# Performance work log

Hardware: AMD Instinct MI355X
Metric: run time of the kernel (lower is better)

The kernel has to match this reference:

```python
import jax, jax.numpy as jnp
import numpy as np

TEMPERATURE = 0.5
B, D = 4096, 256


def setup_inputs() -> dict:
    key = jax.random.key(0)
    k1, k2 = jax.random.split(key)
    z_i = jax.random.normal(k1, (B, D), dtype=jnp.float32)
    z_j = jax.random.normal(k2, (B, D), dtype=jnp.float32)
    return {"z_i": z_i, "z_j": z_j}


def reference(z_i, z_j):
    batch = z_i.shape[0]
    n = 2 * batch
    z = jnp.concatenate([z_i, z_j], axis=0)                      # [2B, D]
    z = z / jnp.linalg.norm(z, axis=1, keepdims=True)            # L2-normalize rows
    # cosine_similarity of unit vectors == dot product -> single GEMM
    sim = jnp.einsum('id,jd->ij', z, z) / TEMPERATURE            # [2B, 2B]
    mask = jnp.eye(n, dtype=bool)
    sim = jnp.where(mask, -jnp.inf, sim)                         # mask self-similarity
    positives = jnp.concatenate(
        [jnp.diagonal(sim, offset=batch), jnp.diagonal(sim, offset=-batch)], axis=0
    )                                                            # [2B]
    loss = -positives + jax.nn.logsumexp(sim, axis=1)            # [2B]
    return loss.mean()
```

## Files before the change

kernel.cpp:

```cpp
#include <hip/hip_runtime.h>
#include <hip/hip_bf16.h>
#include <stdint.h>
#include <stddef.h>


#define B_ROWS 4096
#define D_DIM  256
#define N_ROWS 8192
#define BM 128
#define BN 64

typedef __bf16 bf16;
typedef bf16  bf16x8  __attribute__((ext_vector_type(8)));
typedef bf16  bf16x4  __attribute__((ext_vector_type(4)));
typedef float floatx4 __attribute__((ext_vector_type(4)));

__global__ __launch_bounds__(256) void normalize_kernel(
    const float* __restrict__ z_i, const float* __restrict__ z_j,
    bf16* __restrict__ zn, float* __restrict__ sumexp) {
  const int wave = threadIdx.x >> 6;
  const int lane = threadIdx.x & 63;
  const int row  = blockIdx.x * 4 + wave;
  const float* src = (row < B_ROWS) ? (z_i + (size_t)row * D_DIM)
                                    : (z_j + (size_t)(row - B_ROWS) * D_DIM);
  float4 v = ((const float4*)src)[lane];
  float ss = v.x * v.x + v.y * v.y + v.z * v.z + v.w * v.w;
  #pragma unroll
  for (int m = 1; m < 64; m <<= 1) ss += __shfl_xor(ss, m);
  const float rn = rsqrtf(ss) * 1.6986436f;
  bf16x4 o;
  o[0] = (bf16)(v.x * rn);
  o[1] = (bf16)(v.y * rn);
  o[2] = (bf16)(v.z * rn);
  o[3] = (bf16)(v.w * rn);
  ((bf16x4*)(zn + (size_t)row * D_DIM))[lane] = o;
  if (lane == 0) sumexp[row] = 0.f;
}

__global__ __launch_bounds__(256, 2) void simexp_kernel(
    const bf16* __restrict__ zn, float* __restrict__ sumexp,
    float* __restrict__ pos) {
  __shared__ __align__(16) bf16 Bs[2][BN * D_DIM];

  const int tid   = threadIdx.x;
  const int wave  = tid >> 6;
  const int lane  = tid & 63;
  const int lcol  = lane & 15;
  const int lquad = lane >> 4;
  const int wr = (wave >> 1) * 64;
  const int wc = (wave & 1) * 32;
  const int ri = blockIdx.x >> 3;
  const int cj = blockIdx.x & 7;
  const int row_base = ri * BM;
  const int niter = (ri < 32 && cj >= 6) ? 9 : 8;

  auto jt64 = [&](int t) {
    const int s   = (t == 8) ? 32 : 4 * cj + (t >> 1);
    const int sub = (t == 8) ? (cj - 6) : (t & 1);
    return 2 * ((ri + s) & 63) + sub;
  };

  auto stage = [&](int buf, const bf16* src) {
    #pragma unroll
    for (int it = 0; it < 8; ++it) {
      const int s   = it * 256 + tid;
      const int n   = s >> 5;
      const int kcs = s & 31;
      const int kc  = (kcs & 24) | ((kcs & 7) ^ (n & 7));
      __builtin_amdgcn_global_load_lds(
          (const __attribute__((address_space(1))) unsigned int*)
              (src + (size_t)n * D_DIM + kc * 8),
          (__attribute__((address_space(3))) unsigned int*)&Bs[buf][s * 8],
          16, 0, 0);
    }
  };

  stage(0, zn + (size_t)row_base * D_DIM);
  stage(1, zn + (size_t)(row_base + 64) * D_DIM);
  __syncthreads();

  floatx4 af[4][8];
  {
    const int half = wr >> 6;
    #pragma unroll
    for (int ti = 0; ti < 4; ++ti) {
      const int n = ti * 16 + lcol;
      #pragma unroll
      for (int kq = 0; kq < 8; ++kq) {
        const int kc  = kq * 4 + lquad;
        const int kcs = (kc & 24) | ((kc & 7) ^ (n & 7));
        af[ti][kq] = *(const floatx4*)(&Bs[half][(n * 32 + kcs) * 8]);
      }
    }
  }
  __syncthreads();

  stage(0, zn + (size_t)jt64(0) * BN * D_DIM);

  float rowsum[4][4];
  #pragma unroll
  for (int ti = 0; ti < 4; ++ti)
    #pragma unroll
    for (int r = 0; r < 4; ++r) rowsum[ti][r] = 0.f;

  #pragma unroll 1
  for (int t = 0; t < niter; ++t) {
    __syncthreads();
    if (t + 1 < niter) stage((t + 1) & 1, zn + (size_t)jt64(t + 1) * BN * D_DIM);

    floatx4 acc[4][2];
    #pragma unroll
    for (int ti = 0; ti < 4; ++ti)
      #pragma unroll
      for (int tj = 0; tj < 2; ++tj) acc[ti][tj] = floatx4{0.f, 0.f, 0.f, 0.f};

    const bf16* bbase = &Bs[t & 1][0];
    #pragma unroll
    for (int kq = 0; kq < 8; ++kq) {
      const int kc  = kq * 4 + lquad;
      bf16x8 bfr[2];
      #pragma unroll
      for (int tj = 0; tj < 2; ++tj) {
        const int n   = wc + tj * 16 + lcol;
        const int kcs = (kc & 24) | ((kc & 7) ^ (n & 7));
        bfr[tj] = *(const bf16x8*)(bbase + n * D_DIM + kcs * 8);
      }
      #pragma unroll
      for (int ti = 0; ti < 4; ++ti)
        #pragma unroll
        for (int tj = 0; tj < 2; ++tj)
          acc[ti][tj] = __builtin_amdgcn_mfma_f32_16x16x32_bf16(
              __builtin_bit_cast(bf16x8, af[ti][kq]), bfr[tj], acc[ti][tj],
              0, 0, 0);
    }

    const int s    = (t == 8) ? 32 : 4 * cj + (t >> 1);
    const bool diag = (s == 0);
    const bool posT = (s == 32);
    const int jt = jt64(t);
    const int col_base = jt * BN;
    float colsum[2] = {0.f, 0.f};
    #pragma unroll
    for (int ti = 0; ti < 4; ++ti) {
      #pragma unroll
      for (int tj = 0; tj < 2; ++tj) {
        #pragma unroll
        for (int r = 0; r < 4; ++r) {
          const float v = acc[ti][tj][r];
          float e = __builtin_amdgcn_exp2f(v);
          if (diag || posT) {
            const int rg = row_base + wr + ti * 16 + lquad * 4 + r;
            const int cg = col_base + wc + tj * 16 + lcol;
            if (diag && cg == rg) e = 0.f;
            if (posT && cg == rg + B_ROWS) {
              const float p = v * 0.6931471805599453f;
              pos[rg] = p;
              pos[cg] = p;
            }
          }
          rowsum[ti][r] += e;
          colsum[tj]    += e;
        }
      }
    }

    if (!diag) {
      #pragma unroll
      for (int tj = 0; tj < 2; ++tj) {
        float cs = colsum[tj];
        cs += __shfl_xor(cs, 16);
        cs += __shfl_xor(cs, 32);
        if (lquad == 0)
          atomicAdd(&sumexp[col_base + wc + tj * 16 + lcol], cs);
      }
    }
  }

  #pragma unroll
  for (int ti = 0; ti < 4; ++ti) {
    #pragma unroll
    for (int r = 0; r < 4; ++r) {
      float s2 = rowsum[ti][r];
      s2 += __shfl_xor(s2, 1);
      s2 += __shfl_xor(s2, 2);
      s2 += __shfl_xor(s2, 4);
      s2 += __shfl_xor(s2, 8);
      if (lcol == 0) {
        const int grow = row_base + wr + ti * 16 + lquad * 4 + r;
        atomicAdd(&sumexp[grow], s2);
      }
    }
  }
}

__global__ __launch_bounds__(1024) void reduce_kernel(
    const float* __restrict__ sumexp, const float* __restrict__ pos,
    float* __restrict__ out) {
  __shared__ float ws[16];
  const int tid = threadIdx.x;
  float s = 0.f;
  const float ln2 = 0.6931471805599453f;
  for (int k = tid; k < N_ROWS; k += 1024)
    s += __builtin_amdgcn_logf(sumexp[k]) * ln2 - pos[k];
  #pragma unroll
  for (int m = 1; m < 64; m <<= 1) s += __shfl_xor(s, m);
  const int wave = tid >> 6, lane = tid & 63;
  if (lane == 0) ws[wave] = s;
  __syncthreads();
  if (wave == 0) {
    float t = (lane < 16) ? ws[lane] : 0.f;
    #pragma unroll
    for (int m = 1; m < 16; m <<= 1) t += __shfl_xor(t, m);
    if (lane == 0) out[0] = t * (1.0f / N_ROWS);
  }
}

extern "C" void kernel_launch(void* const* d_in, const int* in_sizes, int n_in,
                              void* d_out, int out_size, void* d_ws,
                              size_t ws_size, hipStream_t stream) {
  const float* z_i = (const float*)d_in[0];
  const float* z_j = (const float*)d_in[1];
  float* out = (float*)d_out;

  bf16* zn = (bf16*)d_ws;
  float* sumexp = (float*)((char*)d_ws + (size_t)N_ROWS * D_DIM * sizeof(bf16));
  float* pos = sumexp + N_ROWS;

  normalize_kernel<<<N_ROWS / 4, 256, 0, stream>>>(z_i, z_j, zn, sumexp);
  simexp_kernel<<<512, 256, 0, stream>>>(zn, sumexp, pos);
  reduce_kernel<<<1, 1024, 0, stream>>>(sumexp, pos, out);
}
```

Baseline: 95.57 us.

## Enlarge column tiles to 128 with 8-wave blocks and phased staging pipeline

Result: faster. 92.55 us (-3.2%).

```diff
diff --git a/kernel.cpp b/kernel.cpp
--- a/kernel.cpp
+++ b/kernel.cpp
@@ -8,7 +8,7 @@
 #define D_DIM  256
 #define N_ROWS 8192
 #define BM 128
-#define BN 64
+#define BN 128
 
 typedef __bf16 bf16;
 typedef bf16  bf16x8  __attribute__((ext_vector_type(8)));
@@ -37,7 +37,7 @@
   if (lane == 0) sumexp[row] = 0.f;
 }
 
-__global__ __launch_bounds__(256, 2) void simexp_kernel(
+__global__ __launch_bounds__(512, 2) void simexp_kernel(
     const bf16* __restrict__ zn, float* __restrict__ sumexp,
     float* __restrict__ pos) {
   __shared__ __align__(16) bf16 Bs[2][BN * D_DIM];
@@ -47,23 +47,18 @@
   const int lane  = tid & 63;
   const int lcol  = lane & 15;
   const int lquad = lane >> 4;
-  const int wr = (wave >> 1) * 64;
-  const int wc = (wave & 1) * 32;
-  const int ri = blockIdx.x >> 3;
-  const int cj = blockIdx.x & 7;
+  const int wr = (wave >> 2) * 64;
+  const int wc = (wave & 3) * 32;
+  const int ri = blockIdx.x >> 2;
+  const int cj = blockIdx.x & 3;
   const int row_base = ri * BM;
-  const int niter = (ri < 32 && cj >= 6) ? 9 : 8;
-
-  auto jt64 = [&](int t) {
-    const int s   = (t == 8) ? 32 : 4 * cj + (t >> 1);
-    const int sub = (t == 8) ? (cj - 6) : (t & 1);
-    return 2 * ((ri + s) & 63) + sub;
-  };
-
-  auto stage = [&](int buf, const bf16* src) {
-    #pragma unroll
-    for (int it = 0; it < 8; ++it) {
-      const int s   = it * 256 + tid;
+  const bool has_tail = (ri < 32 && cj >= 2);
+
+  auto ct_of = [&](int t) { return (ri + 8 * cj + t) & 63; };
+
+  auto stageB = [&](int buf, const bf16* src, int it0, int it1) {
+    for (int it = it0; it < it1; ++it) {
+      const int s   = it * 512 + tid;
       const int n   = s >> 5;
       const int kcs = s & 31;
       const int kc  = (kcs & 24) | ((kcs & 7) ^ (n & 7));
@@ -75,70 +70,94 @@
     }
   };
 
-  stage(0, zn + (size_t)row_base * D_DIM);
-  stage(1, zn + (size_t)(row_base + 64) * D_DIM);
+  stageB(0, zn + (size_t)row_base * D_DIM, 0, 8);
+  stageB(1, zn + (size_t)ct_of(0) * BM * D_DIM, 0, 8);
   __syncthreads();
 
   floatx4 af[4][8];
-  {
-    const int half = wr >> 6;
-    #pragma unroll
-    for (int ti = 0; ti < 4; ++ti) {
-      const int n = ti * 16 + lcol;
-      #pragma unroll
-      for (int kq = 0; kq < 8; ++kq) {
-        const int kc  = kq * 4 + lquad;
-        const int kcs = (kc & 24) | ((kc & 7) ^ (n & 7));
-        af[ti][kq] = *(const floatx4*)(&Bs[half][(n * 32 + kcs) * 8]);
-      }
-    }
-  }
-  __syncthreads();
-
-  stage(0, zn + (size_t)jt64(0) * BN * D_DIM);
-
-  float rowsum[4][4];
-  #pragma unroll
-  for (int ti = 0; ti < 4; ++ti)
-    #pragma unroll
-    for (int r = 0; r < 4; ++r) rowsum[ti][r] = 0.f;
-
-  #pragma unroll 1
-  for (int t = 0; t < niter; ++t) {
-    __syncthreads();
-    if (t + 1 < niter) stage((t + 1) & 1, zn + (size_t)jt64(t + 1) * BN * D_DIM);
-
-    floatx4 acc[4][2];
-    #pragma unroll
-    for (int ti = 0; ti < 4; ++ti)
-      #pragma unroll
-      for (int tj = 0; tj < 2; ++tj) acc[ti][tj] = floatx4{0.f, 0.f, 0.f, 0.f};
-
-    const bf16* bbase = &Bs[t & 1][0];
+  #pragma unroll
+  for (int ti = 0; ti < 4; ++ti) {
+    const int n = wr + ti * 16 + lcol;
     #pragma unroll
     for (int kq = 0; kq < 8; ++kq) {
       const int kc  = kq * 4 + lquad;
-      bf16x8 bfr[2];
-      #pragma unroll
-      for (int tj = 0; tj < 2; ++tj) {
-        const int n   = wc + tj * 16 + lcol;
-        const int kcs = (kc & 24) | ((kc & 7) ^ (n & 7));
-        bfr[tj] = *(const bf16x8*)(bbase + n * D_DIM + kcs * 8);
-      }
-      #pragma unroll
-      for (int ti = 0; ti < 4; ++ti)
-        #pragma unroll
-        for (int tj = 0; tj < 2; ++tj)
-          acc[ti][tj] = __builtin_amdgcn_mfma_f32_16x16x32_bf16(
-              __builtin_bit_cast(bf16x8, af[ti][kq]), bfr[tj], acc[ti][tj],
-              0, 0, 0);
-    }
-
-    const int s    = (t == 8) ? 32 : 4 * cj + (t >> 1);
-    const bool diag = (s == 0);
-    const bool posT = (s == 32);
-    const int jt = jt64(t);
-    const int col_base = jt * BN;
+      const int kcs = (kc & 24) | ((kc & 7) ^ (n & 7));
+      af[ti][kq] = *(const floatx4*)(&Bs[0][(n * 32 + kcs) * 8]);
+    }
+  }
+  __syncthreads();
+
+  float rowsum[4][4];
+  #pragma unroll
+  for (int ti = 0; ti < 4; ++ti)
+    #pragma unroll
+    for (int r = 0; r < 4; ++r) rowsum[ti][r] = 0.f;
+
+#define MFMA_(A, B_, C) __builtin_amdgcn_mfma_f32_16x16x32_bf16( \
+    __builtin_bit_cast(bf16x8, A), B_, C, 0, 0, 0)
+#define PHASE(KQA, KQB, IT0, IT1, DO_VM)                                  \
+  {                                                                       \
+    bf16x8 bfrA[2], bfrB[2];                                              \
+    const int kcA = (KQA) * 4 + lquad, kcB = (KQB) * 4 + lquad;           \
+    _Pragma("unroll")                                                     \
+    for (int tj = 0; tj < 2; ++tj) {                                      \
+      const int n  = wc + tj * 16 + lcol;                                 \
+      const int sA = (kcA & 24) | ((kcA & 7) ^ (n & 7));                  \
+      const int sB = (kcB & 24) | ((kcB & 7) ^ (n & 7));                  \
+      bfrA[tj] = *(const bf16x8*)(bbase + n * D_DIM + sA * 8);            \
+      bfrB[tj] = *(const bf16x8*)(bbase + n * D_DIM + sB * 8);            \
+    }                                                                     \
+    stageB(sb, nsrc, IT0, IT1);                                           \
+    __builtin_amdgcn_sched_barrier(0);                                    \
+    __builtin_amdgcn_s_barrier();                                         \
+    asm volatile("s_waitcnt lgkmcnt(0)" ::: "memory");                    \
+    __builtin_amdgcn_sched_barrier(0);                                    \
+    __builtin_amdgcn_s_setprio(1);                                        \
+    _Pragma("unroll")                                                     \
+    for (int ti = 0; ti < 4; ++ti) {                                      \
+      acc[ti][0] = MFMA_(af[ti][KQA], bfrA[0], acc[ti][0]);               \
+      acc[ti][1] = MFMA_(af[ti][KQA], bfrA[1], acc[ti][1]);               \
+    }                                                                     \
+    _Pragma("unroll")                                                     \
+    for (int ti = 0; ti < 4; ++ti) {                                      \
+      acc[ti][0] = MFMA_(af[ti][KQB], bfrB[0], acc[ti][0]);               \
+      acc[ti][1] = MFMA_(af[ti][KQB], bfrB[1], acc[ti][1]);               \
+    }                                                                     \
+    __builtin_amdgcn_s_setprio(0);                                        \
+    if (DO_VM) asm volatile("s_waitcnt vmcnt(0)" ::: "memory");           \
+    __builtin_amdgcn_sched_barrier(0);                                    \
+    __builtin_amdgcn_s_barrier();                                         \
+  }
+
+  #pragma unroll 1
+  for (int t = 0; t < 8; ++t) {
+    const int cb = (t ^ 1) & 1;
+    const int sb = cb ^ 1;
+    const bf16* bbase = &Bs[cb][0];
+    const bf16* nsrc = nullptr;
+    int nl = 0;
+    if (t < 7) {
+      nsrc = zn + (size_t)ct_of(t + 1) * BM * D_DIM;
+      nl = 8;
+    } else if (has_tail) {
+      nsrc = zn + (size_t)((ri + 32) * BM + (cj - 2) * 64) * D_DIM;
+      nl = 4;
+    }
+    const int nh = nl >> 1;
+
+    floatx4 acc[4][2];
+    #pragma unroll
+    for (int ti = 0; ti < 4; ++ti)
+      #pragma unroll
+      for (int tj = 0; tj < 2; ++tj) acc[ti][tj] = floatx4{0.f, 0.f, 0.f, 0.f};
+
+    PHASE(0, 1, 0, nh, false)
+    PHASE(2, 3, nh, nl, false)
+    PHASE(4, 5, 0, 0, false)
+    PHASE(6, 7, 0, 0, true)
+
+    const bool diag = (cj == 0 && t == 0);
+    const int col_base = ct_of(t) * BM;
     float colsum[2] = {0.f, 0.f};
     #pragma unroll
     for (int ti = 0; ti < 4; ++ti) {
@@ -148,22 +167,16 @@
         for (int r = 0; r < 4; ++r) {
           const float v = acc[ti][tj][r];
           float e = __builtin_amdgcn_exp2f(v);
-          if (diag || posT) {
+          if (diag) {
             const int rg = row_base + wr + ti * 16 + lquad * 4 + r;
             const int cg = col_base + wc + tj * 16 + lcol;
-            if (diag && cg == rg) e = 0.f;
-            if (posT && cg == rg + B_ROWS) {
-              const float p = v * 0.6931471805599453f;
-              pos[rg] = p;
-              pos[cg] = p;
-            }
+            if (cg == rg) e = 0.f;
           }
           rowsum[ti][r] += e;
           colsum[tj]    += e;
         }
       }
     }
-
     if (!diag) {
       #pragma unroll
       for (int tj = 0; tj < 2; ++tj) {
@@ -175,6 +188,64 @@
       }
     }
   }
+
+  if (has_tail && wc < 64) {
+    const int h = cj - 2;
+    const int col_base = (ri + 32) * BM + h * 64;
+    const bf16* bbase = &Bs[1][0];
+    floatx4 acc[4][2];
+    #pragma unroll
+    for (int ti = 0; ti < 4; ++ti)
+      #pragma unroll
+      for (int tj = 0; tj < 2; ++tj) acc[ti][tj] = floatx4{0.f, 0.f, 0.f, 0.f};
+    #pragma unroll
+    for (int kq = 0; kq < 8; ++kq) {
+      const int kc = kq * 4 + lquad;
+      bf16x8 bfr[2];
+      #pragma unroll
+      for (int tj = 0; tj < 2; ++tj) {
+        const int n   = wc + tj * 16 + lcol;
+        const int kcs = (kc & 24) | ((kc & 7) ^ (n & 7));
+        bfr[tj] = *(const bf16x8*)(bbase + n * D_DIM + kcs * 8);
+      }
+      #pragma unroll
+      for (int ti = 0; ti < 4; ++ti) {
+        acc[ti][0] = MFMA_(af[ti][kq], bfr[0], acc[ti][0]);
+        acc[ti][1] = MFMA_(af[ti][kq], bfr[1], acc[ti][1]);
+      }
+    }
+    float colsum[2] = {0.f, 0.f};
+    #pragma unroll
+    for (int ti = 0; ti < 4; ++ti) {
+      #pragma unroll
+      for (int tj = 0; tj < 2; ++tj) {
+        #pragma unroll
+        for (int r = 0; r < 4; ++r) {
+          const float v = acc[ti][tj][r];
+          const float e = __builtin_amdgcn_exp2f(v);
+          const int rg = row_base + wr + ti * 16 + lquad * 4 + r;
+          const int cg = col_base + wc + tj * 16 + lcol;
+          if (cg == rg + B_ROWS) {
+            const float p = v * 0.6931471805599453f;
+            pos[rg] = p;
+            pos[cg] = p;
+          }
+          rowsum[ti][r] += e;
+          colsum[tj]    += e;
+        }
+      }
+    }
+    #pragma unroll
+    for (int tj = 0; tj < 2; ++tj) {
+      float cs = colsum[tj];
+      cs += __shfl_xor(cs, 16);
+      cs += __shfl_xor(cs, 32);
+      if (lquad == 0)
+        atomicAdd(&sumexp[col_base + wc + tj * 16 + lcol], cs);
+    }
+  }
+#undef PHASE
+#undef MFMA_
 
   #pragma unroll
   for (int ti = 0; ti < 4; ++ti) {
@@ -227,6 +298,6 @@
   float* pos = sumexp + N_ROWS;
 
   normalize_kernel<<<N_ROWS / 4, 256, 0, stream>>>(z_i, z_j, zn, sumexp);
-  simexp_kernel<<<512, 256, 0, stream>>>(zn, sumexp, pos);
+  simexp_kernel<<<256, 512, 0, stream>>>(zn, sumexp, pos);
   reduce_kernel<<<1, 1024, 0, stream>>>(sumexp, pos, out);
 }
```

## Use 128x128 tiles with 8 waves and software-pipeline MFMA against exp epilogue

Applied to the files above, without the earlier changes.

Result: faster. 92.08 us (-3.7%).

```diff
diff --git a/kernel.cpp b/kernel.cpp
--- a/kernel.cpp
+++ b/kernel.cpp
@@ -8,7 +8,7 @@
 #define D_DIM  256
 #define N_ROWS 8192
 #define BM 128
-#define BN 64
+#define BN 128
 
 typedef __bf16 bf16;
 typedef bf16  bf16x8  __attribute__((ext_vector_type(8)));
@@ -37,7 +37,7 @@
   if (lane == 0) sumexp[row] = 0.f;
 }
 
-__global__ __launch_bounds__(256, 2) void simexp_kernel(
+__global__ __launch_bounds__(512, 2) void simexp_kernel(
     const bf16* __restrict__ zn, float* __restrict__ sumexp,
     float* __restrict__ pos) {
   __shared__ __align__(16) bf16 Bs[2][BN * D_DIM];
@@ -47,23 +47,18 @@
   const int lane  = tid & 63;
   const int lcol  = lane & 15;
   const int lquad = lane >> 4;
-  const int wr = (wave >> 1) * 64;
-  const int wc = (wave & 1) * 32;
-  const int ri = blockIdx.x >> 3;
-  const int cj = blockIdx.x & 7;
+  const int wr = (wave >> 1) * 32;
+  const int wc = (wave & 1) * 64;
+  const int ri = blockIdx.x >> 2;
+  const int cj = blockIdx.x & 3;
   const int row_base = ri * BM;
-  const int niter = (ri < 32 && cj >= 6) ? 9 : 8;
-
-  auto jt64 = [&](int t) {
-    const int s   = (t == 8) ? 32 : 4 * cj + (t >> 1);
-    const int sub = (t == 8) ? (cj - 6) : (t & 1);
-    return 2 * ((ri + s) & 63) + sub;
-  };
-
-  auto stage = [&](int buf, const bf16* src) {
-    #pragma unroll
-    for (int it = 0; it < 8; ++it) {
-      const int s   = it * 256 + tid;
+  const bool has_tail = (ri < 32 && cj >= 2);
+
+  auto ct_of = [&](int t) { return (ri + 8 * cj + t) & 63; };
+
+  auto stageB = [&](int buf, const bf16* src, int it0, int it1) {
+    for (int it = it0; it < it1; ++it) {
+      const int s   = it * 512 + tid;
       const int n   = s >> 5;
       const int kcs = s & 31;
       const int kc  = (kcs & 24) | ((kcs & 7) ^ (n & 7));
@@ -75,109 +70,142 @@
     }
   };
 
-  stage(0, zn + (size_t)row_base * D_DIM);
-  stage(1, zn + (size_t)(row_base + 64) * D_DIM);
+  stageB(0, zn + (size_t)row_base * D_DIM, 0, 8);
+  stageB(1, zn + (size_t)ct_of(0) * BM * D_DIM, 0, 8);
   __syncthreads();
 
-  floatx4 af[4][8];
-  {
-    const int half = wr >> 6;
-    #pragma unroll
-    for (int ti = 0; ti < 4; ++ti) {
-      const int n = ti * 16 + lcol;
-      #pragma unroll
-      for (int kq = 0; kq < 8; ++kq) {
-        const int kc  = kq * 4 + lquad;
-        const int kcs = (kc & 24) | ((kc & 7) ^ (n & 7));
-        af[ti][kq] = *(const floatx4*)(&Bs[half][(n * 32 + kcs) * 8]);
-      }
-    }
-  }
-  __syncthreads();
-
-  stage(0, zn + (size_t)jt64(0) * BN * D_DIM);
-
-  float rowsum[4][4];
-  #pragma unroll
-  for (int ti = 0; ti < 4; ++ti)
-    #pragma unroll
-    for (int r = 0; r < 4; ++r) rowsum[ti][r] = 0.f;
-
-  #pragma unroll 1
-  for (int t = 0; t < niter; ++t) {
-    __syncthreads();
-    if (t + 1 < niter) stage((t + 1) & 1, zn + (size_t)jt64(t + 1) * BN * D_DIM);
-
-    floatx4 acc[4][2];
-    #pragma unroll
-    for (int ti = 0; ti < 4; ++ti)
-      #pragma unroll
-      for (int tj = 0; tj < 2; ++tj) acc[ti][tj] = floatx4{0.f, 0.f, 0.f, 0.f};
-
-    const bf16* bbase = &Bs[t & 1][0];
+  floatx4 af[2][8];
+  #pragma unroll
+  for (int ti = 0; ti < 2; ++ti) {
+    const int n = wr + ti * 16 + lcol;
     #pragma unroll
     for (int kq = 0; kq < 8; ++kq) {
       const int kc  = kq * 4 + lquad;
-      bf16x8 bfr[2];
+      const int kcs = (kc & 24) | ((kc & 7) ^ (n & 7));
+      af[ti][kq] = *(const floatx4*)(&Bs[0][(n * 32 + kcs) * 8]);
+    }
+  }
+  __syncthreads();
+
+  float rowsum[2][4];
+  #pragma unroll
+  for (int ti = 0; ti < 2; ++ti)
+    #pragma unroll
+    for (int r = 0; r < 4; ++r) rowsum[ti][r] = 0.f;
+
+#define MFMA_(A, B_, C) __builtin_amdgcn_mfma_f32_16x16x32_bf16( \
+    __builtin_bit_cast(bf16x8, A), B_, C, 0, 0, 0)
+
+#define QPHASE(ACC, Q)                                                    \
+  {                                                                       \
+    bf16x8 bfr[8];                                                        \
+    const int n = wc + (Q) * 16 + lcol;                                   \
+    _Pragma("unroll")                                                     \
+    for (int kq = 0; kq < 8; ++kq) {                                      \
+      const int kc  = kq * 4 + lquad;                                     \
+      const int kcs = (kc & 24) | ((kc & 7) ^ (n & 7));                   \
+      bfr[kq] = *(const bf16x8*)(bbase + n * D_DIM + kcs * 8);            \
+    }                                                                     \
+    ACC[0] = floatx4{0.f, 0.f, 0.f, 0.f};                                 \
+    ACC[1] = floatx4{0.f, 0.f, 0.f, 0.f};                                 \
+    _Pragma("unroll")                                                     \
+    for (int kq = 0; kq < 8; ++kq) {                                      \
+      ACC[0] = MFMA_(af[0][kq], bfr[kq], ACC[0]);                         \
+      ACC[1] = MFMA_(af[1][kq], bfr[kq], ACC[1]);                         \
+    }                                                                     \
+  }
+
+#define SLICE(ACC, Q, CB, DG)                                             \
+  {                                                                       \
+    float cs = 0.f;                                                       \
+    _Pragma("unroll")                                                     \
+    for (int ti = 0; ti < 2; ++ti) {                                      \
+      _Pragma("unroll")                                                   \
+      for (int r = 0; r < 4; ++r) {                                       \
+        const float v = ACC[ti][r];                                       \
+        float e = __builtin_amdgcn_exp2f(v);                              \
+        if (DG) {                                                         \
+          const int rg = row_base + wr + ti * 16 + lquad * 4 + r;         \
+          const int cg = (CB) + wc + (Q) * 16 + lcol;                     \
+          if (cg == rg) e = 0.f;                \
+        }                                                                 \
+        rowsum[ti][r] += e;                                               \
+        cs += e;                                                          \
+      }                                                                   \
+    }                                                                     \
+    cs += __shfl_xor(cs, 16);                                             \
+    cs += __shfl_xor(cs, 32);                                             \
+    if (!(DG) && lquad == 0)                                              \
+      atomicAdd(&sumexp[(CB) + wc + (Q) * 16 + lcol], cs);                \
+  }
+
+  floatx4 a3[2];
+  int  pcol3  = 0;
+  bool pdiag3 = false;
+
+  #pragma unroll 1
+  for (int t = 0; t < 8; ++t) {
+    const bf16* bbase = &Bs[(t + 1) & 1][0];
+    const int sb = t & 1;
+    if (t < 7) {
+      stageB(sb, zn + (size_t)ct_of(t + 1) * BM * D_DIM, 0, 8);
+    } else if (has_tail) {
+      stageB(sb, zn + (size_t)((ri + 32) * BM + (cj - 2) * 64) * D_DIM, 0, 4);
+    }
+    const int  colb = ct_of(t) * BM;
+    const bool diag = (cj == 0 && t == 0);
+
+    floatx4 a0[2], a1[2], a2[2];
+    QPHASE(a0, 0)
+    if (t > 0) SLICE(a3, 3, pcol3, pdiag3)
+    QPHASE(a1, 1)
+    SLICE(a0, 0, colb, diag)
+    QPHASE(a2, 2)
+    SLICE(a1, 1, colb, diag)
+    QPHASE(a3, 3)
+    SLICE(a2, 2, colb, diag)
+    pcol3 = colb;
+    pdiag3 = diag;
+    __syncthreads();
+  }
+  SLICE(a3, 3, pcol3, pdiag3)
+
+  if (has_tail && wc == 0) {
+    const int colb = (ri + 32) * BM + (cj - 2) * 64;
+    const bf16* bbase = &Bs[1][0];
+    floatx4 ta[2];
+    #pragma unroll
+    for (int Q = 0; Q < 4; ++Q) {
+      QPHASE(ta, Q)
+      float cs = 0.f;
       #pragma unroll
-      for (int tj = 0; tj < 2; ++tj) {
-        const int n   = wc + tj * 16 + lcol;
-        const int kcs = (kc & 24) | ((kc & 7) ^ (n & 7));
-        bfr[tj] = *(const bf16x8*)(bbase + n * D_DIM + kcs * 8);
-      }
-      #pragma unroll
-      for (int ti = 0; ti < 4; ++ti)
-        #pragma unroll
-        for (int tj = 0; tj < 2; ++tj)
-          acc[ti][tj] = __builtin_amdgcn_mfma_f32_16x16x32_bf16(
-              __builtin_bit_cast(bf16x8, af[ti][kq]), bfr[tj], acc[ti][tj],
-              0, 0, 0);
-    }
-
-    const int s    = (t == 8) ? 32 : 4 * cj + (t >> 1);
-    const bool diag = (s == 0);
-    const bool posT = (s == 32);
-    const int jt = jt64(t);
-    const int col_base = jt * BN;
-    float colsum[2] = {0.f, 0.f};
-    #pragma unroll
-    for (int ti = 0; ti < 4; ++ti) {
-      #pragma unroll
-      for (int tj = 0; tj < 2; ++tj) {
+      for (int ti = 0; ti < 2; ++ti) {
         #pragma unroll
         for (int r = 0; r < 4; ++r) {
-          const float v = acc[ti][tj][r];
-          float e = __builtin_amdgcn_exp2f(v);
-          if (diag || posT) {
-            const int rg = row_base + wr + ti * 16 + lquad * 4 + r;
-            const int cg = col_base + wc + tj * 16 + lcol;
-            if (diag && cg == rg) e = 0.f;
-            if (posT && cg == rg + B_ROWS) {
-              const float p = v * 0.6931471805599453f;
-              pos[rg] = p;
-              pos[cg] = p;
-            }
+          const float v = ta[ti][r];
+          const float e = __builtin_amdgcn_exp2f(v);
+          const int rg = row_base + wr + ti * 16 + lquad * 4 + r;
+          const int cg = colb + Q * 16 + lcol;
+          if (cg == rg + B_ROWS) {
+            const float p = v * 0.6931471805599453f;
+            pos[rg] = p;
+            pos[cg] = p;
           }
           rowsum[ti][r] += e;
-          colsum[tj]    += e;
+          cs += e;
         }
       }
-    }
-
-    if (!diag) {
-      #pragma unroll
-      for (int tj = 0; tj < 2; ++tj) {
-        float cs = colsum[tj];
-        cs += __shfl_xor(cs, 16);
-        cs += __shfl_xor(cs, 32);
-        if (lquad == 0)
-          atomicAdd(&sumexp[col_base + wc + tj * 16 + lcol], cs);
-      }
-    }
-  }
-
-  #pragma unroll
-  for (int ti = 0; ti < 4; ++ti) {
+      cs += __shfl_xor(cs, 16);
+      cs += __shfl_xor(cs, 32);
+      if (lquad == 0) atomicAdd(&sumexp[colb + Q * 16 + lcol], cs);
+    }
+  }
+#undef SLICE
+#undef QPHASE
+#undef MFMA_
+
+  #pragma unroll
+  for (int ti = 0; ti < 2; ++ti) {
     #pragma unroll
     for (int r = 0; r < 4; ++r) {
       float s2 = rowsum[ti][r];
@@ -227,6 +255,6 @@
   float* pos = sumexp + N_ROWS;
 
   normalize_kernel<<<N_ROWS / 4, 256, 0, stream>>>(z_i, z_j, zn, sumexp);
-  simexp_kernel<<<512, 256, 0, stream>>>(zn, sumexp, pos);
+  simexp_kernel<<<256, 512, 0, stream>>>(zn, sumexp, pos);
   reduce_kernel<<<1, 1024, 0, stream>>>(sumexp, pos, out);
 }
```

## Split block tile across eight waves with smaller per-wave A fragment

Applied to the files above, without the earlier changes.

Result: no change. 95.49 us (-0.1%).

```diff
diff --git a/kernel.cpp b/kernel.cpp
--- a/kernel.cpp
+++ b/kernel.cpp
@@ -37,7 +37,7 @@
   if (lane == 0) sumexp[row] = 0.f;
 }
 
-__global__ __launch_bounds__(256, 2) void simexp_kernel(
+__global__ __launch_bounds__(512, 4) void simexp_kernel(
     const bf16* __restrict__ zn, float* __restrict__ sumexp,
     float* __restrict__ pos) {
   __shared__ __align__(16) bf16 Bs[2][BN * D_DIM];
@@ -47,7 +47,7 @@
   const int lane  = tid & 63;
   const int lcol  = lane & 15;
   const int lquad = lane >> 4;
-  const int wr = (wave >> 1) * 64;
+  const int wr = (wave >> 1) * 32;
   const int wc = (wave & 1) * 32;
   const int ri = blockIdx.x >> 3;
   const int cj = blockIdx.x & 7;
@@ -60,10 +60,10 @@
     return 2 * ((ri + s) & 63) + sub;
   };
 
-  auto stage = [&](int buf, const bf16* src) {
-    #pragma unroll
-    for (int it = 0; it < 8; ++it) {
-      const int s   = it * 256 + tid;
+  auto stageB = [&](int buf, const bf16* src) {
+    #pragma unroll
+    for (int it = 0; it < 4; ++it) {
+      const int s   = it * 512 + tid;
       const int n   = s >> 5;
       const int kcs = s & 31;
       const int kc  = (kcs & 24) | ((kcs & 7) ^ (n & 7));
@@ -75,82 +75,71 @@
     }
   };
 
-  stage(0, zn + (size_t)row_base * D_DIM);
-  stage(1, zn + (size_t)(row_base + 64) * D_DIM);
+  stageB(0, zn + (size_t)row_base * D_DIM);
+  stageB(1, zn + (size_t)(row_base + 64) * D_DIM);
   __syncthreads();
 
-  floatx4 af[4][8];
-  {
-    const int half = wr >> 6;
-    #pragma unroll
-    for (int ti = 0; ti < 4; ++ti) {
-      const int n = ti * 16 + lcol;
+  floatx4 af[2][8];
+  #pragma unroll
+  for (int ti = 0; ti < 2; ++ti) {
+    const int n    = wr + ti * 16 + lcol;
+    const int half = n >> 6;
+    const int nl   = n & 63;
+    #pragma unroll
+    for (int kq = 0; kq < 8; ++kq) {
+      const int kc  = kq * 4 + lquad;
+      const int kcs = (kc & 24) | ((kc & 7) ^ (nl & 7));
+      af[ti][kq] = *(const floatx4*)(&Bs[half][(nl * 32 + kcs) * 8]);
+    }
+  }
+  __syncthreads();
+
+  stageB(0, zn + (size_t)jt64(0) * BN * D_DIM);
+
+  float rowsum[2][4];
+  #pragma unroll
+  for (int ti = 0; ti < 2; ++ti)
+    #pragma unroll
+    for (int r = 0; r < 4; ++r) rowsum[ti][r] = 0.f;
+
+#define MFMA_(A, B_, C) __builtin_amdgcn_mfma_f32_16x16x32_bf16( \
+    __builtin_bit_cast(bf16x8, A), B_, C, 0, 0, 0)
+
+  #pragma unroll 1
+  for (int t = 0; t < niter; ++t) {
+    __syncthreads();
+    if (t + 1 < niter) stageB((t + 1) & 1, zn + (size_t)jt64(t + 1) * BN * D_DIM);
+
+    const bf16* bbase = &Bs[t & 1][0];
+    const int s    = (t == 8) ? 32 : 4 * cj + (t >> 1);
+    const bool diag = (s == 0);
+    const bool posT = (s == 32);
+    const int colb = jt64(t) * BN;
+
+    #pragma unroll
+    for (int Q = 0; Q < 2; ++Q) {
+      const int n = wc + Q * 16 + lcol;
+      floatx4 acc[2];
+      acc[0] = floatx4{0.f, 0.f, 0.f, 0.f};
+      acc[1] = floatx4{0.f, 0.f, 0.f, 0.f};
       #pragma unroll
       for (int kq = 0; kq < 8; ++kq) {
         const int kc  = kq * 4 + lquad;
         const int kcs = (kc & 24) | ((kc & 7) ^ (n & 7));
-        af[ti][kq] = *(const floatx4*)(&Bs[half][(n * 32 + kcs) * 8]);
+        const bf16x8 b = *(const bf16x8*)(bbase + n * D_DIM + kcs * 8);
+        acc[0] = MFMA_(af[0][kq], b, acc[0]);
+        acc[1] = MFMA_(af[1][kq], b, acc[1]);
       }
-    }
-  }
-  __syncthreads();
-
-  stage(0, zn + (size_t)jt64(0) * BN * D_DIM);
-
-  float rowsum[4][4];
-  #pragma unroll
-  for (int ti = 0; ti < 4; ++ti)
-    #pragma unroll
-    for (int r = 0; r < 4; ++r) rowsum[ti][r] = 0.f;
-
-  #pragma unroll 1
-  for (int t = 0; t < niter; ++t) {
-    __syncthreads();
-    if (t + 1 < niter) stage((t + 1) & 1, zn + (size_t)jt64(t + 1) * BN * D_DIM);
-
-    floatx4 acc[4][2];
-    #pragma unroll
-    for (int ti = 0; ti < 4; ++ti)
+      float cs = 0.f;
       #pragma unroll
-      for (int tj = 0; tj < 2; ++tj) acc[ti][tj] = floatx4{0.f, 0.f, 0.f, 0.f};
-
-    const bf16* bbase = &Bs[t & 1][0];
-    #pragma unroll
-    for (int kq = 0; kq < 8; ++kq) {
-      const int kc  = kq * 4 + lquad;
-      bf16x8 bfr[2];
-      #pragma unroll
-      for (int tj = 0; tj < 2; ++tj) {
-        const int n   = wc + tj * 16 + lcol;
-        const int kcs = (kc & 24) | ((kc & 7) ^ (n & 7));
-        bfr[tj] = *(const bf16x8*)(bbase + n * D_DIM + kcs * 8);
-      }
-      #pragma unroll
-      for (int ti = 0; ti < 4; ++ti)
-        #pragma unroll
-        for (int tj = 0; tj < 2; ++tj)
-          acc[ti][tj] = __builtin_amdgcn_mfma_f32_16x16x32_bf16(
-              __builtin_bit_cast(bf16x8, af[ti][kq]), bfr[tj], acc[ti][tj],
-              0, 0, 0);
-    }
-
-    const int s    = (t == 8) ? 32 : 4 * cj + (t >> 1);
-    const bool diag = (s == 0);
-    const bool posT = (s == 32);
-    const int jt = jt64(t);
-    const int col_base = jt * BN;
-    float colsum[2] = {0.f, 0.f};
-    #pragma unroll
-    for (int ti = 0; ti < 4; ++ti) {
-      #pragma unroll
-      for (int tj = 0; tj < 2; ++tj) {
+      for (int ti = 0; ti < 2; ++ti) {
         #pragma unroll
         for (int r = 0; r < 4; ++r) {
-          const float v = acc[ti][tj][r];
+          const float v = acc[ti][r];
           float e = __builtin_amdgcn_exp2f(v);
           if (diag || posT) {
             const int rg = row_base + wr + ti * 16 + lquad * 4 + r;
-            const int cg = col_base + wc + tj * 16 + lcol;
+            const int cg = colb + wc + Q * 16 + lcol;
             if (diag && cg == rg) e = 0.f;
             if (posT && cg == rg + B_ROWS) {
               const float p = v * 0.6931471805599453f;
@@ -159,25 +148,19 @@
             }
           }
           rowsum[ti][r] += e;
-          colsum[tj]    += e;
+          cs += e;
         }
       }
-    }
-
-    if (!diag) {
-      #pragma unroll
-      for (int tj = 0; tj < 2; ++tj) {
-        float cs = colsum[tj];
-        cs += __shfl_xor(cs, 16);
-        cs += __shfl_xor(cs, 32);
-        if (lquad == 0)
-          atomicAdd(&sumexp[col_base + wc + tj * 16 + lcol], cs);
-      }
-    }
-  }
-
-  #pragma unroll
-  for (int ti = 0; ti < 4; ++ti) {
+      cs += __shfl_xor(cs, 16);
+      cs += __shfl_xor(cs, 32);
+      if (!diag && lquad == 0)
+        atomicAdd(&sumexp[colb + wc + Q * 16 + lcol], cs);
+    }
+  }
+#undef MFMA_
+
+  #pragma unroll
+  for (int ti = 0; ti < 2; ++ti) {
     #pragma unroll
     for (int r = 0; r < 4; ++r) {
       float s2 = rowsum[ti][r];
@@ -227,6 +210,6 @@
   float* pos = sumexp + N_ROWS;
 
   normalize_kernel<<<N_ROWS / 4, 256, 0, stream>>>(z_i, z_j, zn, sumexp);
-  simexp_kernel<<<512, 256, 0, stream>>>(zn, sumexp, pos);
+  simexp_kernel<<<512, 512, 0, stream>>>(zn, sumexp, pos);
   reduce_kernel<<<1, 1024, 0, stream>>>(sumexp, pos, out);
 }
```
